# Kernel tuning notes

Hardware: AMD Instinct MI355X
Metric: run time of the kernel (lower is better)

The kernel has to match this reference:

```python
import jax, jax.numpy as jnp
import numpy as np

P = 2
N_BINS = 15
NUM_CLASSES = 100
N_SRC = 500_000
N_TGT = 500_000


def setup_inputs() -> dict:
    key = jax.random.key(0)
    k1, k2, k3, k4 = jax.random.split(key, 4)
    logits_source = jax.random.normal(k1, (N_SRC, NUM_CLASSES), dtype=jnp.float32)
    labels_source = jax.random.randint(k2, (N_SRC,), 0, NUM_CLASSES, dtype=jnp.int64)
    logits_target = jax.random.normal(k3, (N_TGT, NUM_CLASSES), dtype=jnp.float32)
    weight = jax.random.uniform(k4, (NUM_CLASSES,), dtype=jnp.float32)
    return {"logits_source": logits_source, "labels_source": labels_source,
            "logits_target": logits_target, "weight": weight}


def _equal_mass_edges(conf_target):
    # histedges_equalN: interp(linspace(0, N, n_bins+1), arange(N), sort(conf))
    n = conf_target.shape[0]
    srt = jnp.sort(conf_target)
    xq = jnp.linspace(0.0, float(n), N_BINS + 1)
    xp = jnp.arange(n, dtype=conf_target.dtype)
    return jnp.interp(xq, xp, srt)


def reference(logits_source, labels_source, logits_target, weight):
    sm_s = jax.nn.softmax(logits_source, axis=1)
    sm_t = jax.nn.softmax(logits_target, axis=1)
    conf_s = jnp.max(sm_s, axis=1)              # [Ns]
    pred_s = jnp.argmax(sm_s, axis=1)           # [Ns]
    conf_t = jnp.max(sm_t, axis=1)              # [Nt]
    n_s = conf_s.shape[0]
    n_t = conf_t.shape[0]

    edges = jax.lax.stop_gradient(_equal_mass_edges(conf_t))  # bins from numpy in original
    lo = edges[:-1][:, None]  # [B,1]
    hi = edges[1:][:, None]   # [B,1]

    in_s = (conf_s[None, :] > lo) & (conf_s[None, :] <= hi)   # [B, Ns] bool
    in_t = (conf_t[None, :] > lo) & (conf_t[None, :] <= hi)   # [B, Nt] bool

    acc = (pred_s == labels_source)                           # [Ns] bool
    # per-sample weighted accuracy: weights[label_i] * acc_i
    w_per = weight[labels_source] * acc.astype(weight.dtype)  # [Ns]

    weighted_num = jnp.einsum('bn,n->b', in_s.astype(w_per.dtype), w_per)  # [B]
    count_t = jnp.sum(in_t, axis=1)                                        # [B] int

    normalizer = (n_t - 1) / n_s
    denom = jnp.maximum(count_t - 1, 1).astype(weighted_num.dtype)
    cond_expect = normalizer * weighted_num / denom                        # [B]

    diff_p = jnp.abs(conf_t[None, :] - cond_expect[:, None]) ** P          # [B, Nt]
    per_bin = jnp.sum(in_t.astype(diff_p.dtype) * diff_p, axis=1)          # [B]
    per_bin = jnp.where(count_t > 1, per_bin, 0.0)

    return (jnp.sum(per_bin) / n_t)[None]  # shape [1], matches torch output
```

## Files before the change

kernel.cpp:

```cpp
#include <hip/hip_runtime.h>
#include <math.h>

typedef unsigned int u32;

#define NROWS 500000
#define NCLS  100
#define NBINS 15
#define NRANK 31
#define NSLOT 32
#define TROWS 64
#define HISTB 128

#define NEG_INF (-__builtin_inff())

#define OFF_CONF_T 0
#define OFF_CONF_S 2000000
#define OFF_WPER   4000000
#define OFF_CHIST  6000128
#define OFF_SHIST  (OFF_CHIST + 262144)
#define OFF_ACC    (OFF_SHIST + 8388608)
#define OFF_SMAP   (OFF_ACC + 256)
#define OFF_ZEND   (OFF_SMAP + 262144)
#define OFF_META   OFF_ZEND
#define OFF_VALS   (OFF_META + 512)
#define OFF_EDGES  (OFF_VALS + 128)
#define OFF_CE     (OFF_EDGES + 128)

__global__ __launch_bounds__(256) void zero_kernel(u32* __restrict__ p, int n) {
    int i = blockIdx.x * 256 + threadIdx.x;
    if (i < n) p[i] = 0u;
}

__global__ __launch_bounds__(256) void conf_kernel(
    const float* __restrict__ logits_t, const float* __restrict__ logits_s,
    const int* __restrict__ labels, const float* __restrict__ weight,
    float* __restrict__ conf_t, float* __restrict__ conf_s,
    float* __restrict__ wper, int tb)
{
    __shared__ __align__(16) float tile[TROWS * NCLS];
    int t = threadIdx.x;
    bool is_src = (int)blockIdx.x >= tb;
    int bid = is_src ? (int)blockIdx.x - tb : (int)blockIdx.x;
    const float* logits = is_src ? logits_s : logits_t;
    int tile0 = bid * TROWS;
    int rows = NROWS - tile0; if (rows > TROWS) rows = TROWS;
    const float4* gp = (const float4*)(logits + (size_t)tile0 * NCLS);
    int wv = t >> 6, ln = t & 63;

    if (rows == TROWS) {
        #pragma unroll
        for (int k = 0; k < 7; ++k) {
            int idx = k * 256 + wv * 64 + ln;
            if (idx < TROWS * 25) {
                __builtin_amdgcn_global_load_lds(
                    (const __attribute__((address_space(1))) u32*)(gp + idx),
                    (__attribute__((address_space(3))) u32*)(&tile[(k * 256 + wv * 64) * 4]),
                    16, 0, 0);
            }
        }
    } else {
        int nf4 = rows * 25;
        for (int idx = t; idx < nf4; idx += 256) {
            float4 v = gp[idx];
            *(float4*)&tile[idx * 4] = v;
        }
    }
    __syncthreads();

    int r = t >> 2, qd = t & 3;
    const float* rp = &tile[r * NCLS];
    float4 x[7];
    #pragma unroll
    for (int k = 0; k < 6; ++k)
        x[k] = *(const float4*)(rp + (qd + 4 * k) * 4);
    x[6] = (qd == 0) ? *(const float4*)(rp + 96)
                     : make_float4(NEG_INF, NEG_INF, NEG_INF, NEG_INF);

    float4 m4 = x[0];
    #pragma unroll
    for (int k = 1; k < 7; ++k) {
        m4.x = fmaxf(m4.x, x[k].x); m4.y = fmaxf(m4.y, x[k].y);
        m4.z = fmaxf(m4.z, x[k].z); m4.w = fmaxf(m4.w, x[k].w);
    }
    float m = fmaxf(fmaxf(m4.x, m4.y), fmaxf(m4.z, m4.w));
    m = fmaxf(m, __shfl_xor(m, 1));
    m = fmaxf(m, __shfl_xor(m, 2));

    float sx = 0.f, sy = 0.f, sz = 0.f, sw = 0.f;
    #pragma unroll
    for (int k = 0; k < 7; ++k) {
        sx += __expf(x[k].x - m); sy += __expf(x[k].y - m);
        sz += __expf(x[k].z - m); sw += __expf(x[k].w - m);
    }
    float s = (sx + sy) + (sz + sw);
    s += __shfl_xor(s, 1);
    s += __shfl_xor(s, 2);

    if (qd == 0 && r < rows) {
        float c = 1.0f / s;
        int row = tile0 + r;
        if (is_src) {
            conf_s[row] = c;
            int lab = labels[row];
            wper[row] = (rp[lab] == m) ? weight[lab] : 0.0f;
        } else {
            conf_t[row] = c;
        }
    }
}

__global__ __launch_bounds__(256) void hist_kernel(
    const float* __restrict__ conf, u32* __restrict__ chist)
{
    __shared__ u32 h[1024];
    int t = threadIdx.x;
    for (int i = t; i < 1024; i += 256) h[i] = 0u;
    __syncthreads();
    for (int i = blockIdx.x * 256 + t; i < NROWS; i += HISTB * 256) {
        u32 b = __float_as_uint(conf[i]) >> 16;
        u32 u = b - 15360u;
        if (u < 1024u) atomicAdd(&h[u], 1u);
        else atomicAdd(&chist[b], 1u);
    }
    __syncthreads();
    for (int i = t; i < 1024; i += 256) {
        u32 v = h[i];
        if (v) atomicAdd(&chist[15360 + i], v);
    }
}

__device__ __forceinline__ int rank_of(int q) {
    if (q == NRANK - 1) return NROWS - 1;
    int k = q >> 1;
    int ik = (int)(((long long)k * 100000) / 3);
    return ik + (q & 1);
}

__global__ __launch_bounds__(1024) void rank_prep_kernel(
    const u32* __restrict__ chist, int* __restrict__ smap, int* __restrict__ meta)
{
    __shared__ u32 pre[1024];
    __shared__ u32 wtot[16];
    __shared__ int s_cq[NRANK], s_res[NRANK], s_bin[NRANK];
    __shared__ u32 cd[NRANK * 64];
    __shared__ int s_slotbin[NSLOT];
    __shared__ int s_ns;
    int t = threadIdx.x;
    const uint4* hp = (const uint4*)chist;
    u32 csum = 0;
    for (int j = 0; j < 16; ++j) { uint4 v = hp[t * 16 + j]; csum += v.x + v.y + v.z + v.w; }
    u32 x = csum;
    for (int off = 1; off < 64; off <<= 1) { u32 y = __shfl_up(x, off); if ((t & 63) >= off) x += y; }
    int wv = t >> 6;
    if ((t & 63) == 63) wtot[wv] = x;
    __syncthreads();
    if (t == 0) { u32 run = 0; for (int w = 0; w < 16; ++w) { u32 v = wtot[w]; wtot[w] = run; run += v; } }
    __syncthreads();
    pre[t] = x - csum + wtot[wv];
    __syncthreads();
    if (t < NRANK) {
        u32 r = (u32)rank_of(t);
        int lo = 0, hi = 1023;
        while (lo < hi) { int mid = (lo + hi + 1) >> 1; if (pre[mid] <= r) lo = mid; else hi = mid - 1; }
        s_cq[t] = lo;
        s_res[t] = (int)(r - pre[lo]);
    }
    __syncthreads();
    for (int idx = t; idx < NRANK * 64; idx += 1024) {
        int q = idx >> 6, j = idx & 63;
        cd[idx] = chist[s_cq[q] * 64 + j];
    }
    __syncthreads();
    if (t < NRANK) {
        u32 run = 0; u32 res = (u32)s_res[t]; int bin = 0;
        for (int j = 0; j < 64; ++j) {
            u32 h = cd[t * 64 + j];
            if (res < run + h) { bin = s_cq[t] * 64 + j; s_res[t] = (int)(res - run); break; }
            run += h;
        }
        s_bin[t] = bin;
    }
    __syncthreads();
    if (t == 0) {
        int ns = 0;
        for (int q = 0; q < NRANK; ++q) {
            int b = s_bin[q], sl = -1;
            for (int u = 0; u < ns; ++u) if (s_slotbin[u] == b) { sl = u; break; }
            if (sl < 0) { sl = ns; s_slotbin[ns++] = b; }
            meta[q] = b; meta[32 + q] = s_res[q]; meta[64 + q] = sl;
        }
        s_ns = ns; meta[96] = ns;
    }
    __syncthreads();
    if (t < s_ns) smap[s_slotbin[t]] = t + 1;
}

__global__ __launch_bounds__(256) void slot_hist_kernel(
    const float* __restrict__ conf, const int* __restrict__ smap, u32* __restrict__ shist)
{
    int i = blockIdx.x * 256 + threadIdx.x;
    if (i >= NROWS) return;
    u32 b = __float_as_uint(conf[i]);
    int sl = smap[b >> 16] - 1;
    if (sl >= 0) atomicAdd(&shist[(size_t)sl * 65536 + (b & 0xFFFFu)], 1u);
}

__global__ __launch_bounds__(1024) void select_kernel(
    const u32* __restrict__ shist, const int* __restrict__ meta, float* __restrict__ vals)
{
    __shared__ u32 wtot[16];
    __shared__ int s_chunk; __shared__ u32 s_base;
    __shared__ u32 cd[64];
    int q = blockIdx.x, t = threadIdx.x;
    int sl = meta[64 + q]; u32 res = (u32)meta[32 + q]; int bin = meta[q];
    const u32* h = shist + (size_t)sl * 65536;
    const uint4* hp = (const uint4*)h;
    u32 csum = 0;
    for (int j = 0; j < 16; ++j) { uint4 v = hp[t * 16 + j]; csum += v.x + v.y + v.z + v.w; }
    u32 x = csum;
    for (int off = 1; off < 64; off <<= 1) { u32 y = __shfl_up(x, off); if ((t & 63) >= off) x += y; }
    int wv = t >> 6;
    if ((t & 63) == 63) wtot[wv] = x;
    __syncthreads();
    if (t == 0) { u32 run = 0; for (int w = 0; w < 16; ++w) { u32 v = wtot[w]; wtot[w] = run; run += v; } }
    __syncthreads();
    u32 prex = x - csum + wtot[wv];
    if (res >= prex && res < prex + csum) { s_chunk = t; s_base = prex; }
    __syncthreads();
    int c = s_chunk;
    if (t < 64) cd[t] = h[c * 64 + t];
    __syncthreads();
    if (t == 0) {
        u32 run = s_base; int low = 0;
        for (int j = 0; j < 64; ++j) {
            u32 hh = cd[j];
            if (res < run + hh) { low = c * 64 + j; break; }
            run += hh;
        }
        vals[q] = __uint_as_float(((u32)bin << 16) | (u32)low);
    }
}

__global__ void edges_kernel(const float* __restrict__ vals, double* __restrict__ edges,
                             float* __restrict__ fedges) {
    int k = threadIdx.x;
    if (k < 16) {
        double e;
        if (k == 0)       e = (double)vals[0];
        else if (k == 15) e = (double)vals[30];
        else {
            double step = (double)NROWS / 15.0;
            long long ik = ((long long)k * 100000) / 3;
            double frac = (double)k * step - (double)ik;
            double a = (double)vals[2 * k];
            double b = (double)vals[2 * k + 1];
            e = a + frac * (b - a);
        }
        edges[k] = e;
        float f = (float)e;
        if ((double)f > e) f = __uint_as_float(__float_as_uint(f) - 1u);
        fedges[k] = f;
    }
}

__global__ __launch_bounds__(256) void bin_accum_kernel(
    const float* __restrict__ conf_s, const float* __restrict__ wper,
    const float* __restrict__ conf_t, const float* __restrict__ fedges,
    float* __restrict__ g_wnum, int* __restrict__ g_cnt)
{
    __shared__ float l_w[NBINS];
    __shared__ int   l_c[NBINS];
    int t = threadIdx.x;
    if (t < NBINS) { l_w[t] = 0.0f; l_c[t] = 0; }
    __syncthreads();
    float e[16];
    #pragma unroll
    for (int j = 0; j < 16; ++j) e[j] = fedges[j];
    int i = blockIdx.x * 256 + t;
    if (i < NROWS) {
        float c = conf_s[i];
        int cnt = 0;
        #pragma unroll
        for (int j = 0; j < 16; ++j) cnt += (c > e[j]) ? 1 : 0;
        if (cnt >= 1 && cnt <= NBINS) {
            float w = wper[i];
            if (w != 0.0f) atomicAdd(&l_w[cnt - 1], w);
        }
    } else if (i < 2 * NROWS) {
        float c = conf_t[i - NROWS];
        int cnt = 0;
        #pragma unroll
        for (int j = 0; j < 16; ++j) cnt += (c > e[j]) ? 1 : 0;
        if (cnt >= 1 && cnt <= NBINS) atomicAdd(&l_c[cnt - 1], 1);
    }
    __syncthreads();
    if (t < NBINS) {
        float w = l_w[t];
        int cc = l_c[t];
        if (w != 0.0f) atomicAdd(&g_wnum[t], w);
        if (cc) atomicAdd(&g_cnt[t], cc);
    }
}

__global__ void cond_kernel(const float* __restrict__ g_wnum, const int* __restrict__ g_cnt,
                            double* __restrict__ ce)
{
    int t = threadIdx.x;
    if (t < NBINS) {
        int d = g_cnt[t] - 1; if (d < 1) d = 1;
        ce[t] = ((double)(NROWS - 1) / (double)NROWS) * (double)g_wnum[t] / (double)d;
    }
}

__global__ __launch_bounds__(256) void diff_kernel(
    const float* __restrict__ conf_t, const float* __restrict__ fedges,
    const double* __restrict__ ce, float* __restrict__ g_perbin)
{
    __shared__ float l_p[NBINS];
    int t = threadIdx.x;
    if (t < NBINS) l_p[t] = 0.0f;
    __syncthreads();
    float e[16];
    #pragma unroll
    for (int j = 0; j < 16; ++j) e[j] = fedges[j];
    int i = blockIdx.x * 256 + t;
    if (i < NROWS) {
        float c = conf_t[i];
        int cnt = 0;
        #pragma unroll
        for (int j = 0; j < 16; ++j) cnt += (c > e[j]) ? 1 : 0;
        if (cnt >= 1 && cnt <= NBINS) {
            double d = (double)c - ce[cnt - 1];
            atomicAdd(&l_p[cnt - 1], (float)(d * d));
        }
    }
    __syncthreads();
    if (t < NBINS) {
        float p = l_p[t];
        if (p != 0.0f) atomicAdd(&g_perbin[t], p);
    }
}

__global__ void final_kernel(const float* __restrict__ g_perbin, const int* __restrict__ g_cnt,
                             float* __restrict__ out)
{
    if (threadIdx.x == 0 && blockIdx.x == 0) {
        double ssum = 0.0;
        for (int b = 0; b < NBINS; ++b)
            if (g_cnt[b] > 1) ssum += (double)g_perbin[b];
        out[0] = (float)(ssum / (double)NROWS);
    }
}

extern "C" void kernel_launch(void* const* d_in, const int* in_sizes, int n_in,
                              void* d_out, int out_size, void* d_ws, size_t ws_size,
                              hipStream_t stream)
{
    const float* logits_s = (const float*)d_in[0];
    const int*   labels   = (const int*)d_in[1];
    const float* logits_t = (const float*)d_in[2];
    const float* weight   = (const float*)d_in[3];

    char* ws = (char*)d_ws;
    float*  conf_t   = (float*)(ws + OFF_CONF_T);
    float*  conf_s   = (float*)(ws + OFF_CONF_S);
    float*  wper     = (float*)(ws + OFF_WPER);
    u32*    chist    = (u32*)(ws + OFF_CHIST);
    u32*    shist    = (u32*)(ws + OFF_SHIST);
    int*    smap     = (int*)(ws + OFF_SMAP);
    int*    meta     = (int*)(ws + OFF_META);
    float*  vals     = (float*)(ws + OFF_VALS);
    double* edges    = (double*)(ws + OFF_EDGES);
    double* ce       = (double*)(ws + OFF_CE);
    float*  g_wnum   = (float*)(ws + OFF_ACC);
    int*    g_cnt    = (int*)(ws + OFF_ACC + 64);
    float*  g_perbin = (float*)(ws + OFF_ACC + 128);
    float*  fedges   = (float*)(ws + OFF_ACC + 192);
    float*  out      = (float*)d_out;

    int zwords = (OFF_ZEND - OFF_CHIST) / 4;
    zero_kernel<<<(zwords + 255) / 256, 256, 0, stream>>>((u32*)(ws + OFF_CHIST), zwords);

    int tb = (NROWS + TROWS - 1) / TROWS;
    int gb = (NROWS + 255) / 256;
    conf_kernel<<<2 * tb, 256, 0, stream>>>(logits_t, logits_s, labels, weight,
                                            conf_t, conf_s, wper, tb);
    hist_kernel<<<HISTB, 256, 0, stream>>>(conf_t, chist);
    rank_prep_kernel<<<1, 1024, 0, stream>>>(chist, smap, meta);
    slot_hist_kernel<<<gb, 256, 0, stream>>>(conf_t, smap, shist);
    select_kernel<<<NRANK, 1024, 0, stream>>>(shist, meta, vals);
    edges_kernel<<<1, 64, 0, stream>>>(vals, edges, fedges);
    bin_accum_kernel<<<(2 * NROWS + 255) / 256, 256, 0, stream>>>(conf_s, wper, conf_t, fedges, g_wnum, g_cnt);
    cond_kernel<<<1, 64, 0, stream>>>(g_wnum, g_cnt, ce);
    diff_kernel<<<gb, 256, 0, stream>>>(conf_t, fedges, ce, g_perbin);
    final_kernel<<<1, 64, 0, stream>>>(g_perbin, g_cnt, out);
}
```

Measured before the change: 527.1 us.

## Fuse small serial kernels via last-block counters and drop LDS staging in conf

Merges the histogram with rank prep, select with edge computation, bin accumulation with cond, and diff with final reduction. Each pair is joined by an atomic last-block-done counter, which removes four kernel launches and their gaps. The conf kernel now loads logits straight from global memory into registers instead of staging them through LDS with global_load_lds, and sets an occupancy hint. This cuts launch and synchronisation overhead, but the direct loads are less coalesced and the counters add threadfence and atomic traffic.

```diff
diff --git a/kernel.cpp b/kernel.cpp
--- a/kernel.cpp
+++ b/kernel.cpp
@@ -1,5 +1,4 @@
 #include <hip/hip_runtime.h>
-#include <math.h>
 
 typedef unsigned int u32;
 
@@ -9,7 +8,7 @@
 #define NRANK 31
 #define NSLOT 32
 #define TROWS 64
-#define HISTB 128
+#define HRB   32
 
 #define NEG_INF (-__builtin_inff())
 
@@ -19,61 +18,37 @@
 #define OFF_CHIST  6000128
 #define OFF_SHIST  (OFF_CHIST + 262144)
 #define OFF_ACC    (OFF_SHIST + 8388608)
-#define OFF_SMAP   (OFF_ACC + 256)
+#define OFF_SMAP   (OFF_ACC + 384)
 #define OFF_ZEND   (OFF_SMAP + 262144)
 #define OFF_META   OFF_ZEND
 #define OFF_VALS   (OFF_META + 512)
-#define OFF_EDGES  (OFF_VALS + 128)
-#define OFF_CE     (OFF_EDGES + 128)
+#define OFF_CE     (OFF_VALS + 128)
 
 __global__ __launch_bounds__(256) void zero_kernel(u32* __restrict__ p, int n) {
     int i = blockIdx.x * 256 + threadIdx.x;
     if (i < n) p[i] = 0u;
 }
 
-__global__ __launch_bounds__(256) void conf_kernel(
+__global__ __launch_bounds__(256, 8) void conf_kernel(
     const float* __restrict__ logits_t, const float* __restrict__ logits_s,
     const int* __restrict__ labels, const float* __restrict__ weight,
     float* __restrict__ conf_t, float* __restrict__ conf_s,
     float* __restrict__ wper, int tb)
 {
-    __shared__ __align__(16) float tile[TROWS * NCLS];
     int t = threadIdx.x;
     bool is_src = (int)blockIdx.x >= tb;
     int bid = is_src ? (int)blockIdx.x - tb : (int)blockIdx.x;
     const float* logits = is_src ? logits_s : logits_t;
-    int tile0 = bid * TROWS;
-    int rows = NROWS - tile0; if (rows > TROWS) rows = TROWS;
-    const float4* gp = (const float4*)(logits + (size_t)tile0 * NCLS);
-    int wv = t >> 6, ln = t & 63;
-
-    if (rows == TROWS) {
-        #pragma unroll
-        for (int k = 0; k < 7; ++k) {
-            int idx = k * 256 + wv * 64 + ln;
-            if (idx < TROWS * 25) {
-                __builtin_amdgcn_global_load_lds(
-                    (const __attribute__((address_space(1))) u32*)(gp + idx),
-                    (__attribute__((address_space(3))) u32*)(&tile[(k * 256 + wv * 64) * 4]),
-                    16, 0, 0);
-            }
-        }
-    } else {
-        int nf4 = rows * 25;
-        for (int idx = t; idx < nf4; idx += 256) {
-            float4 v = gp[idx];
-            *(float4*)&tile[idx * 4] = v;
-        }
-    }
-    __syncthreads();
-
     int r = t >> 2, qd = t & 3;
-    const float* rp = &tile[r * NCLS];
+    int row = bid * TROWS + r;
+    int lrow = row < NROWS ? row : NROWS - 1;
+    const float4* rp4 = (const float4*)(logits + (size_t)lrow * NCLS);
+
     float4 x[7];
     #pragma unroll
     for (int k = 0; k < 6; ++k)
-        x[k] = *(const float4*)(rp + (qd + 4 * k) * 4);
-    x[6] = (qd == 0) ? *(const float4*)(rp + 96)
+        x[k] = rp4[qd + 4 * k];
+    x[6] = (qd == 0) ? rp4[24]
                      : make_float4(NEG_INF, NEG_INF, NEG_INF, NEG_INF);
 
     float4 m4 = x[0];
@@ -96,36 +71,16 @@
     s += __shfl_xor(s, 1);
     s += __shfl_xor(s, 2);
 
-    if (qd == 0 && r < rows) {
+    if (qd == 0 && row < NROWS) {
         float c = 1.0f / s;
-        int row = tile0 + r;
         if (is_src) {
             conf_s[row] = c;
             int lab = labels[row];
-            wper[row] = (rp[lab] == m) ? weight[lab] : 0.0f;
+            float lv = logits[(size_t)row * NCLS + lab];
+            wper[row] = (lv == m) ? weight[lab] : 0.0f;
         } else {
             conf_t[row] = c;
         }
-    }
-}
-
-__global__ __launch_bounds__(256) void hist_kernel(
-    const float* __restrict__ conf, u32* __restrict__ chist)
-{
-    __shared__ u32 h[1024];
-    int t = threadIdx.x;
-    for (int i = t; i < 1024; i += 256) h[i] = 0u;
-    __syncthreads();
-    for (int i = blockIdx.x * 256 + t; i < NROWS; i += HISTB * 256) {
-        u32 b = __float_as_uint(conf[i]) >> 16;
-        u32 u = b - 15360u;
-        if (u < 1024u) atomicAdd(&h[u], 1u);
-        else atomicAdd(&chist[b], 1u);
-    }
-    __syncthreads();
-    for (int i = t; i < 1024; i += 256) {
-        u32 v = h[i];
-        if (v) atomicAdd(&chist[15360 + i], v);
     }
 }
 
@@ -136,16 +91,36 @@
     return ik + (q & 1);
 }
 
-__global__ __launch_bounds__(1024) void rank_prep_kernel(
-    const u32* __restrict__ chist, int* __restrict__ smap, int* __restrict__ meta)
-{
+__global__ __launch_bounds__(1024) void hist_rank_kernel(
+    const float* __restrict__ conf, u32* __restrict__ chist,
+    int* __restrict__ smap, int* __restrict__ meta, u32* __restrict__ ctr)
+{
+    __shared__ u32 h[1024];
+    __shared__ int s_last;
+    int t = threadIdx.x;
+    h[t] = 0u;
+    __syncthreads();
+    for (int i = blockIdx.x * 1024 + t; i < NROWS; i += HRB * 1024) {
+        u32 b = __float_as_uint(conf[i]) >> 16;
+        u32 u = b - 15360u;
+        if (u < 1024u) atomicAdd(&h[u], 1u);
+        else atomicAdd(&chist[b], 1u);
+    }
+    __syncthreads();
+    { u32 v = h[t]; if (v) atomicAdd(&chist[15360 + t], v); }
+    __threadfence();
+    __syncthreads();
+    if (t == 0) s_last = (atomicAdd(ctr, 1u) == HRB - 1) ? 1 : 0;
+    __syncthreads();
+    if (!s_last) return;
+    __threadfence();
+
     __shared__ u32 pre[1024];
     __shared__ u32 wtot[16];
     __shared__ int s_cq[NRANK], s_res[NRANK], s_bin[NRANK];
     __shared__ u32 cd[NRANK * 64];
     __shared__ int s_slotbin[NSLOT];
     __shared__ int s_ns;
-    int t = threadIdx.x;
     const uint4* hp = (const uint4*)chist;
     u32 csum = 0;
     for (int j = 0; j < 16; ++j) { uint4 v = hp[t * 16 + j]; csum += v.x + v.y + v.z + v.w; }
@@ -174,9 +149,9 @@
     if (t < NRANK) {
         u32 run = 0; u32 res = (u32)s_res[t]; int bin = 0;
         for (int j = 0; j < 64; ++j) {
-            u32 h = cd[t * 64 + j];
-            if (res < run + h) { bin = s_cq[t] * 64 + j; s_res[t] = (int)(res - run); break; }
-            run += h;
+            u32 hh = cd[t * 64 + j];
+            if (res < run + hh) { bin = s_cq[t] * 64 + j; s_res[t] = (int)(res - run); break; }
+            run += hh;
         }
         s_bin[t] = bin;
     }
@@ -205,12 +180,14 @@
     if (sl >= 0) atomicAdd(&shist[(size_t)sl * 65536 + (b & 0xFFFFu)], 1u);
 }
 
-__global__ __launch_bounds__(1024) void select_kernel(
-    const u32* __restrict__ shist, const int* __restrict__ meta, float* __restrict__ vals)
+__global__ __launch_bounds__(1024) void select_edges_kernel(
+    const u32* __restrict__ shist, const int* __restrict__ meta,
+    float* __restrict__ vals, float* __restrict__ fedges, u32* __restrict__ ctr)
 {
     __shared__ u32 wtot[16];
     __shared__ int s_chunk; __shared__ u32 s_base;
     __shared__ u32 cd[64];
+    __shared__ int s_last;
     int q = blockIdx.x, t = threadIdx.x;
     int sl = meta[64 + q]; u32 res = (u32)meta[32 + q]; int bin = meta[q];
     const u32* h = shist + (size_t)sl * 65536;
@@ -238,13 +215,14 @@
             run += hh;
         }
         vals[q] = __uint_as_float(((u32)bin << 16) | (u32)low);
-    }
-}
-
-__global__ void edges_kernel(const float* __restrict__ vals, double* __restrict__ edges,
-                             float* __restrict__ fedges) {
-    int k = threadIdx.x;
-    if (k < 16) {
+        __threadfence();
+        s_last = (atomicAdd(ctr, 1u) == NRANK - 1) ? 1 : 0;
+    }
+    __syncthreads();
+    if (!s_last) return;
+    __threadfence();
+    if (t < 16) {
+        int k = t;
         double e;
         if (k == 0)       e = (double)vals[0];
         else if (k == 15) e = (double)vals[30];
@@ -256,20 +234,21 @@
             double b = (double)vals[2 * k + 1];
             e = a + frac * (b - a);
         }
-        edges[k] = e;
         float f = (float)e;
         if ((double)f > e) f = __uint_as_float(__float_as_uint(f) - 1u);
         fedges[k] = f;
     }
 }
 
-__global__ __launch_bounds__(256) void bin_accum_kernel(
+__global__ __launch_bounds__(256) void bin_cond_kernel(
     const float* __restrict__ conf_s, const float* __restrict__ wper,
     const float* __restrict__ conf_t, const float* __restrict__ fedges,
-    float* __restrict__ g_wnum, int* __restrict__ g_cnt)
+    float* __restrict__ g_wnum, int* __restrict__ g_cnt,
+    double* __restrict__ ce, u32* __restrict__ ctr, int nblocks)
 {
     __shared__ float l_w[NBINS];
     __shared__ int   l_c[NBINS];
+    __shared__ int   s_last;
     int t = threadIdx.x;
     if (t < NBINS) { l_w[t] = 0.0f; l_c[t] = 0; }
     __syncthreads();
@@ -300,23 +279,26 @@
         if (w != 0.0f) atomicAdd(&g_wnum[t], w);
         if (cc) atomicAdd(&g_cnt[t], cc);
     }
-}
-
-__global__ void cond_kernel(const float* __restrict__ g_wnum, const int* __restrict__ g_cnt,
-                            double* __restrict__ ce)
-{
-    int t = threadIdx.x;
+    __threadfence();
+    __syncthreads();
+    if (t == 0) s_last = (atomicAdd(ctr, 1u) == (u32)(nblocks - 1)) ? 1 : 0;
+    __syncthreads();
+    if (!s_last) return;
+    __threadfence();
     if (t < NBINS) {
         int d = g_cnt[t] - 1; if (d < 1) d = 1;
         ce[t] = ((double)(NROWS - 1) / (double)NROWS) * (double)g_wnum[t] / (double)d;
     }
 }
 
-__global__ __launch_bounds__(256) void diff_kernel(
+__global__ __launch_bounds__(256) void diff_final_kernel(
     const float* __restrict__ conf_t, const float* __restrict__ fedges,
-    const double* __restrict__ ce, float* __restrict__ g_perbin)
+    const double* __restrict__ ce, float* __restrict__ g_perbin,
+    const int* __restrict__ g_cnt, float* __restrict__ out,
+    u32* __restrict__ ctr, int nblocks)
 {
     __shared__ float l_p[NBINS];
+    __shared__ int   s_last;
     int t = threadIdx.x;
     if (t < NBINS) l_p[t] = 0.0f;
     __syncthreads();
@@ -339,12 +321,13 @@
         float p = l_p[t];
         if (p != 0.0f) atomicAdd(&g_perbin[t], p);
     }
-}
-
-__global__ void final_kernel(const float* __restrict__ g_perbin, const int* __restrict__ g_cnt,
-                             float* __restrict__ out)
-{
-    if (threadIdx.x == 0 && blockIdx.x == 0) {
+    __threadfence();
+    __syncthreads();
+    if (t == 0) s_last = (atomicAdd(ctr, 1u) == (u32)(nblocks - 1)) ? 1 : 0;
+    __syncthreads();
+    if (!s_last) return;
+    __threadfence();
+    if (t == 0) {
         double ssum = 0.0;
         for (int b = 0; b < NBINS; ++b)
             if (g_cnt[b] > 1) ssum += (double)g_perbin[b];
@@ -370,12 +353,12 @@
     int*    smap     = (int*)(ws + OFF_SMAP);
     int*    meta     = (int*)(ws + OFF_META);
     float*  vals     = (float*)(ws + OFF_VALS);
-    double* edges    = (double*)(ws + OFF_EDGES);
     double* ce       = (double*)(ws + OFF_CE);
     float*  g_wnum   = (float*)(ws + OFF_ACC);
     int*    g_cnt    = (int*)(ws + OFF_ACC + 64);
     float*  g_perbin = (float*)(ws + OFF_ACC + 128);
     float*  fedges   = (float*)(ws + OFF_ACC + 192);
+    u32*    ctrs     = (u32*)(ws + OFF_ACC + 256);
     float*  out      = (float*)d_out;
 
     int zwords = (OFF_ZEND - OFF_CHIST) / 4;
@@ -383,15 +366,14 @@
 
     int tb = (NROWS + TROWS - 1) / TROWS;
     int gb = (NROWS + 255) / 256;
+    int nb2 = (2 * NROWS + 255) / 256;
     conf_kernel<<<2 * tb, 256, 0, stream>>>(logits_t, logits_s, labels, weight,
                                             conf_t, conf_s, wper, tb);
-    hist_kernel<<<HISTB, 256, 0, stream>>>(conf_t, chist);
-    rank_prep_kernel<<<1, 1024, 0, stream>>>(chist, smap, meta);
+    hist_rank_kernel<<<HRB, 1024, 0, stream>>>(conf_t, chist, smap, meta, &ctrs[0]);
     slot_hist_kernel<<<gb, 256, 0, stream>>>(conf_t, smap, shist);
-    select_kernel<<<NRANK, 1024, 0, stream>>>(shist, meta, vals);
-    edges_kernel<<<1, 64, 0, stream>>>(vals, edges, fedges);
-    bin_accum_kernel<<<(2 * NROWS + 255) / 256, 256, 0, stream>>>(conf_s, wper, conf_t, fedges, g_wnum, g_cnt);
-    cond_kernel<<<1, 64, 0, stream>>>(g_wnum, g_cnt, ce);
-    diff_kernel<<<gb, 256, 0, stream>>>(conf_t, fedges, ce, g_perbin);
-    final_kernel<<<1, 64, 0, stream>>>(g_perbin, g_cnt, out);
-}
+    select_edges_kernel<<<NRANK, 1024, 0, stream>>>(shist, meta, vals, fedges, &ctrs[1]);
+    bin_cond_kernel<<<nb2, 256, 0, stream>>>(conf_s, wper, conf_t, fedges,
+                                             g_wnum, g_cnt, ce, &ctrs[2], nb2);
+    diff_final_kernel<<<gb, 256, 0, stream>>>(conf_t, fedges, ce, g_perbin,
+                                              g_cnt, out, &ctrs[3], gb);
+}
```

New measurement: 822.7 us. 1.56x slower.
